# Kernel optimization log

Measured on AMD Instinct MI355X. Metric: run time of the kernel, lower is better.

The kernel has to match this reference:

```python
import jax, jax.numpy as jnp
import numpy as np

UNITS = 400
FEAT = 3
B, T = 128, 1000


def setup_inputs() -> dict:
    key = jax.random.key(0)
    ks = jax.random.split(key, 8)
    s = 0.08  # small init scale
    return {
        "x": jax.random.normal(ks[0], (B, T, FEAT), dtype=jnp.float32),
        "W": jax.random.normal(ks[1], (FEAT, 4 * UNITS), dtype=jnp.float32) * s,
        "U": jax.random.normal(ks[2], (UNITS, 4 * UNITS), dtype=jnp.float32) * s,
        "b": jnp.zeros((4 * UNITS,), dtype=jnp.float32),
        "p_i": jax.random.normal(ks[3], (UNITS,), dtype=jnp.float32) * s,
        "p_f": jax.random.normal(ks[4], (UNITS,), dtype=jnp.float32) * s,
        "p_o": jax.random.normal(ks[5], (UNITS,), dtype=jnp.float32) * s,
        "Wd": jax.random.normal(ks[6], (UNITS, FEAT), dtype=jnp.float32) * s,
        "bd": jnp.zeros((FEAT,), dtype=jnp.float32),
    }


def reference(x, W, U, b, p_i, p_f, p_o, Wd, bd):
    """Peephole LSTM (Graves) scan + dense projection.

    Gate order i, f, g(cell candidate), o. Peepholes: i,f see c_{t-1}; o sees c_t.
    """
    batch = x.shape[0]
    units = U.shape[0]
    # Precompute input contribution for all timesteps: [B, T, 4U]
    xw = jnp.einsum("btf,fg->btg", x, W) + b

    def step(carry, xw_t):
        h, c = carry  # [B, U] each
        z = xw_t + h @ U  # [B, 4U]
        zi, zf, zg, zo = jnp.split(z, 4, axis=-1)
        i = jax.nn.sigmoid(zi + p_i * c)
        f = jax.nn.sigmoid(zf + p_f * c)
        c_new = f * c + i * jnp.tanh(zg)
        o = jax.nn.sigmoid(zo + p_o * c_new)
        h_new = o * jnp.tanh(c_new)
        return (h_new, c_new), h_new

    init = (jnp.zeros((batch, units), x.dtype), jnp.zeros((batch, units), x.dtype))
    _, hs = jax.lax.scan(step, init, jnp.swapaxes(xw, 0, 1))  # hs: [T, B, U]
    hs = jnp.swapaxes(hs, 0, 1)  # [B, T, U]
    return hs @ Wd + bd  # [B, T, FEAT]
```

## Files before the change

kernel.cpp:

```cpp
#include <hip/hip_runtime.h>
#include <hip/hip_bf16.h>

#define UNITS   400
#define BATCH   128
#define TSTEPS  1000
#define NFEAT   3
#define GATES   1600
#define KCAP    448
#define HSTR    456
#define NGROUP  8
#define CWG     20
#define SU      20
#define NCOLS   80
#define ROWS    16
#define NW      5
#define NTHR    320

typedef __bf16 bf16x8 __attribute__((ext_vector_type(8)));
typedef float  v4f    __attribute__((ext_vector_type(4)));

__device__ __forceinline__ float sigm(float v)     { return 1.f / (1.f + __expf(-v)); }
__device__ __forceinline__ float tanhfast(float v) { return 1.f - 2.f / (1.f + __expf(2.f * v)); }

__device__ __forceinline__ unsigned short f2bf(float v) {
    __hip_bfloat16 h = __float2bfloat16(v);
    return *reinterpret_cast<unsigned short*>(&h);
}

__global__ void hw_init_kernel(const float* __restrict__ U, const float* __restrict__ W,
                               const float* __restrict__ b, const float* __restrict__ bd,
                               unsigned short* __restrict__ Urep, float* __restrict__ Wrep,
                               float* __restrict__ brep, unsigned short* __restrict__ Hbuf,
                               int* __restrict__ flags, float* __restrict__ out)
{
    int idx = blockIdx.x * 256 + threadIdx.x;
    if (idx < GATES * KCAP) {
        int col = idx / KCAP, k = idx - col * KCAP;
        int u = col >> 2, G = col & 3;
        float v = (k < UNITS) ? U[k * GATES + G * UNITS + u] : 0.f;
        Urep[idx] = f2bf(v);
        return;
    }
    idx -= GATES * KCAP;
    if (idx < 3 * GATES) {
        int f = idx / GATES, col = idx - f * GATES;
        int u = col >> 2, G = col & 3;
        Wrep[idx] = W[f * GATES + G * UNITS + u];
        return;
    }
    idx -= 3 * GATES;
    if (idx < GATES) {
        int u = idx >> 2, G = idx & 3;
        brep[idx] = b[G * UNITS + u];
        return;
    }
    idx -= GATES;
    if (idx < BATCH * KCAP) { Hbuf[idx] = 0; return; }
    idx -= BATCH * KCAP;
    if (idx < 256) { flags[idx] = 0; return; }
    idx -= 256;
    if (idx < BATCH * TSTEPS * NFEAT) { out[idx] = bd[idx % 3]; return; }
}

__global__ __launch_bounds__(NTHR) void lstm_kernel(
    const float* __restrict__ x,
    const float* __restrict__ p_i, const float* __restrict__ p_f, const float* __restrict__ p_o,
    const float* __restrict__ Wd,
    const unsigned short* __restrict__ Urep,
    const float* __restrict__ Wrep, const float* __restrict__ brep,
    unsigned short* __restrict__ Hbuf,
    int* __restrict__ flags,
    float* __restrict__ out)
{
    __shared__ __align__(16) unsigned short Hl[ROWS * HSTR];
    __shared__ float Wl[3 * NCOLS];
    __shared__ float bl[NCOLS];
    __shared__ float xl[ROWS * 4];
    __shared__ float redw[NW * ROWS * 4];
    float* zb = (float*)Hl;

    const int tid  = threadIdx.x;
    const int lane = tid & 63, wid = tid >> 6;
    const int bid  = blockIdx.x;
    const int grp  = bid & 7;
    const int c    = bid >> 3;
    const int b0   = grp * ROWS;
    const int u0   = c * SU;
    const int col0 = u0 * 4;

    bf16x8 barr[13];
    {
        const int bcol = col0 + wid * 16 + (lane & 15);
        const unsigned short* up = Urep + (size_t)bcol * KCAP + ((lane >> 4) * 8);
        #pragma unroll
        for (int kt = 0; kt < 13; ++kt)
            barr[kt] = *(const bf16x8*)(up + kt * 32);
    }
    for (int i = tid; i < 3 * NCOLS; i += NTHR) {
        int f = i / NCOLS, cl = i - f * NCOLS;
        Wl[i] = Wrep[f * GATES + col0 + cl];
    }
    for (int i = tid; i < NCOLS; i += NTHR) bl[i] = brep[col0 + i];

    const int u   = tid >> 4;
    const int row = tid & 15;
    const int gu  = u0 + u;
    const int gb  = b0 + row;
    const float pi = p_i[gu], pf = p_f[gu], po = p_o[gu];
    const float wd0 = Wd[gu * 3 + 0], wd1 = Wd[gu * 3 + 1], wd2 = Wd[gu * 3 + 2];
    float cst = 0.f;
    int* flagp = flags + grp * 32;

    __syncthreads();

    #pragma unroll 1
    for (int t = 0; t < TSTEPS; ++t) {
        {
            const unsigned long long* src =
                (const unsigned long long*)(Hbuf + (size_t)b0 * KCAP);
            for (int i = tid; i < ROWS * 112; i += NTHR) {
                unsigned long long v = __hip_atomic_load(src + i, __ATOMIC_RELAXED, __HIP_MEMORY_SCOPE_AGENT);
                int r = i / 112, j = i - r * 112;
                *(unsigned long long*)((char*)Hl + r * (HSTR * 2) + j * 8) = v;
            }
            if (tid < 48) {
                int r = tid / 3, f = tid - r * 3;
                xl[r * 4 + f] = x[(size_t)(b0 + r) * (TSTEPS * NFEAT) + t * NFEAT + f];
            }
        }
        __syncthreads();

        v4f acc = {0.f, 0.f, 0.f, 0.f};
        {
            const char* ap = (const char*)Hl + (lane & 15) * (HSTR * 2) + (lane >> 4) * 16;
            #pragma unroll
            for (int kt = 0; kt < 13; ++kt) {
                bf16x8 a = *(const bf16x8*)(ap + kt * 64);
                acc = __builtin_amdgcn_mfma_f32_16x16x32_bf16(a, barr[kt], acc, 0, 0, 0);
            }
        }
        __syncthreads();
        {
            int zc = wid * 16 + (lane & 15);
            int zr = (lane >> 4) * 4;
            #pragma unroll
            for (int j = 0; j < 4; ++j) zb[(zr + j) * NCOLS + zc] = acc[j];
        }
        __syncthreads();

        {
            float x0 = xl[row * 4 + 0], x1 = xl[row * 4 + 1], x2 = xl[row * 4 + 2];
            float z[4];
            #pragma unroll
            for (int G = 0; G < 4; ++G) {
                int cc = u * 4 + G;
                z[G] = zb[row * NCOLS + cc] + bl[cc]
                     + x0 * Wl[0 * NCOLS + cc] + x1 * Wl[1 * NCOLS + cc] + x2 * Wl[2 * NCOLS + cc];
            }
            float iv = sigm(z[0] + pi * cst);
            float fv = sigm(z[1] + pf * cst);
            float cn = fv * cst + iv * tanhfast(z[2]);
            float ov = sigm(z[3] + po * cn);
            float h  = ov * tanhfast(cn);
            cst = cn;

            int hb = (int)f2bf(h);
            int h1 = __shfl_down(hb, 16);
            int h2 = __shfl_down(hb, 32);
            int h3 = __shfl_down(hb, 48);
            if (lane < 16) {
                unsigned int lo = (unsigned int)(hb & 0xffff) | ((unsigned int)(h1 & 0xffff) << 16);
                unsigned int hi = (unsigned int)(h2 & 0xffff) | ((unsigned int)(h3 & 0xffff) << 16);
                unsigned long long pk = (unsigned long long)lo | ((unsigned long long)hi << 32);
                __hip_atomic_store(
                    (unsigned long long*)(Hbuf + (size_t)(b0 + lane) * KCAP + u0 + wid * 4),
                    pk, __ATOMIC_RELAXED, __HIP_MEMORY_SCOPE_AGENT);
            }

            float s0 = h * wd0, s1 = h * wd1, s2 = h * wd2;
            s0 += __shfl_xor(s0, 16); s0 += __shfl_xor(s0, 32);
            s1 += __shfl_xor(s1, 16); s1 += __shfl_xor(s1, 32);
            s2 += __shfl_xor(s2, 16); s2 += __shfl_xor(s2, 32);
            if (lane < 16) {
                redw[(wid * ROWS + lane) * 4 + 0] = s0;
                redw[(wid * ROWS + lane) * 4 + 1] = s1;
                redw[(wid * ROWS + lane) * 4 + 2] = s2;
            }
        }
        __syncthreads();
        if (tid < 48) {
            int f = tid >> 4, r = tid & 15;
            float s = 0.f;
            #pragma unroll
            for (int w2 = 0; w2 < NW; ++w2) s += redw[(w2 * ROWS + r) * 4 + f];
            atomicAdd(&out[(size_t)(b0 + r) * (TSTEPS * NFEAT) + t * NFEAT + f], s);
        }
        __syncthreads();

        if (tid == 0) {
            __hip_atomic_fetch_add(flagp, 1, __ATOMIC_RELAXED, __HIP_MEMORY_SCOPE_AGENT);
            const int target = CWG * (t + 1);
            while (__hip_atomic_load(flagp, __ATOMIC_RELAXED, __HIP_MEMORY_SCOPE_AGENT) < target)
                __builtin_amdgcn_s_sleep(2);
        }
        __syncthreads();
    }
}

extern "C" void kernel_launch(void* const* d_in, const int* in_sizes, int n_in,
                              void* d_out, int out_size, void* d_ws, size_t ws_size,
                              hipStream_t stream)
{
    const float* x   = (const float*)d_in[0];
    const float* W   = (const float*)d_in[1];
    const float* U   = (const float*)d_in[2];
    const float* b   = (const float*)d_in[3];
    const float* p_i = (const float*)d_in[4];
    const float* p_f = (const float*)d_in[5];
    const float* p_o = (const float*)d_in[6];
    const float* Wd  = (const float*)d_in[7];
    const float* bd  = (const float*)d_in[8];
    float* out = (float*)d_out;

    char* p = (char*)d_ws;
    unsigned short* Urep = (unsigned short*)p;  p += (size_t)GATES * KCAP * 2;
    float* Wrep = (float*)p;                    p += (size_t)3 * GATES * 4;
    float* brep = (float*)p;                    p += (size_t)GATES * 4;
    unsigned short* Hbuf = (unsigned short*)p;  p += (size_t)BATCH * KCAP * 2;
    int* flags = (int*)p;                       p += 256 * 4;

    const int total = GATES * KCAP + 3 * GATES + GATES + BATCH * KCAP + 256 + BATCH * TSTEPS * NFEAT;
    const int iblocks = (total + 255) / 256;
    hipLaunchKernelGGL(hw_init_kernel, dim3(iblocks), dim3(256), 0, stream,
                       U, W, b, bd, Urep, Wrep, brep, Hbuf, flags, out);

    hipLaunchKernelGGL(lstm_kernel, dim3(NGROUP * CWG), dim3(NTHR), 0, stream,
                       x, p_i, p_f, p_o, Wd, Urep, Wrep, brep, Hbuf, flags, out);
}
```

Baseline: 3.477 ms.

## Use single-wave blocks with per-wave flags, double-buffered hidden state, and partial output slices

```diff
diff --git a/kernel.cpp b/kernel.cpp
--- a/kernel.cpp
+++ b/kernel.cpp
@@ -4,20 +4,18 @@
 #define UNITS   400
 #define BATCH   128
 #define TSTEPS  1000
-#define NFEAT   3
 #define GATES   1600
 #define KCAP    448
-#define HSTR    456
 #define NGROUP  8
-#define CWG     20
-#define SU      20
-#define NCOLS   80
+#define WPG     100
 #define ROWS    16
-#define NW      5
-#define NTHR    320
+#define OUTSZ   (BATCH*TSTEPS*3)
+#define NSLICE  5
+#define SPIN_GUARD 8192
 
 typedef __bf16 bf16x8 __attribute__((ext_vector_type(8)));
-typedef float  v4f    __attribute__((ext_vector_type(4)));
+typedef float  f32x4  __attribute__((ext_vector_type(4)));
+typedef unsigned long long ull;
 
 __device__ __forceinline__ float sigm(float v)     { return 1.f / (1.f + __expf(-v)); }
 __device__ __forceinline__ float tanhfast(float v) { return 1.f - 2.f / (1.f + __expf(2.f * v)); }
@@ -28,10 +26,10 @@
 }
 
 __global__ void hw_init_kernel(const float* __restrict__ U, const float* __restrict__ W,
-                               const float* __restrict__ b, const float* __restrict__ bd,
+                               const float* __restrict__ b,
                                unsigned short* __restrict__ Urep, float* __restrict__ Wrep,
                                float* __restrict__ brep, unsigned short* __restrict__ Hbuf,
-                               int* __restrict__ flags, float* __restrict__ out)
+                               int* __restrict__ flags, float* __restrict__ outP)
 {
     int idx = blockIdx.x * 256 + threadIdx.x;
     if (idx < GATES * KCAP) {
@@ -55,14 +53,18 @@
         return;
     }
     idx -= GATES;
-    if (idx < BATCH * KCAP) { Hbuf[idx] = 0; return; }
-    idx -= BATCH * KCAP;
-    if (idx < 256) { flags[idx] = 0; return; }
-    idx -= 256;
-    if (idx < BATCH * TSTEPS * NFEAT) { out[idx] = bd[idx % 3]; return; }
-}
-
-__global__ __launch_bounds__(NTHR) void lstm_kernel(
+    if (idx < 2 * BATCH * KCAP) { Hbuf[idx] = 0; return; }
+    idx -= 2 * BATCH * KCAP;
+    if (idx < NGROUP * 128) { flags[idx] = 0; return; }
+    idx -= NGROUP * 128;
+    if (idx < NSLICE * OUTSZ) { outP[idx] = 0.f; return; }
+}
+
+#define LDA(i, offlit) \
+    asm volatile("global_load_dwordx4 %0, %1, off offset:" offlit " sc0 sc1" \
+                 : "=v"(af[i]) : "v"(ab) : "memory");
+
+__global__ __launch_bounds__(64) void lstm_kernel(
     const float* __restrict__ x,
     const float* __restrict__ p_i, const float* __restrict__ p_f, const float* __restrict__ p_o,
     const float* __restrict__ Wd,
@@ -70,141 +72,151 @@
     const float* __restrict__ Wrep, const float* __restrict__ brep,
     unsigned short* __restrict__ Hbuf,
     int* __restrict__ flags,
-    float* __restrict__ out)
-{
-    __shared__ __align__(16) unsigned short Hl[ROWS * HSTR];
-    __shared__ float Wl[3 * NCOLS];
-    __shared__ float bl[NCOLS];
-    __shared__ float xl[ROWS * 4];
-    __shared__ float redw[NW * ROWS * 4];
-    float* zb = (float*)Hl;
-
-    const int tid  = threadIdx.x;
-    const int lane = tid & 63, wid = tid >> 6;
+    float* __restrict__ outP)
+{
+    const int lane = threadIdx.x;
     const int bid  = blockIdx.x;
     const int grp  = bid & 7;
-    const int c    = bid >> 3;
+    const int widx = bid >> 3;
     const int b0   = grp * ROWS;
-    const int u0   = c * SU;
-    const int col0 = u0 * 4;
+    const int ub   = widx * 4;
+    const int col0 = widx * 16;
+    const int row  = lane & 15;
+    const int kg   = lane >> 4;
+    const int gu   = ub + kg;
 
     bf16x8 barr[13];
     {
-        const int bcol = col0 + wid * 16 + (lane & 15);
-        const unsigned short* up = Urep + (size_t)bcol * KCAP + ((lane >> 4) * 8);
+        const unsigned short* up = Urep + (size_t)(col0 + row) * KCAP + kg * 8;
         #pragma unroll
         for (int kt = 0; kt < 13; ++kt)
             barr[kt] = *(const bf16x8*)(up + kt * 32);
     }
-    for (int i = tid; i < 3 * NCOLS; i += NTHR) {
-        int f = i / NCOLS, cl = i - f * NCOLS;
-        Wl[i] = Wrep[f * GATES + col0 + cl];
-    }
-    for (int i = tid; i < NCOLS; i += NTHR) bl[i] = brep[col0 + i];
-
-    const int u   = tid >> 4;
-    const int row = tid & 15;
-    const int gu  = u0 + u;
-    const int gb  = b0 + row;
+
+    float w0[4], w1[4], w2[4], bz[4];
+    #pragma unroll
+    for (int G = 0; G < 4; ++G) {
+        w0[G] = Wrep[0 * GATES + gu * 4 + G];
+        w1[G] = Wrep[1 * GATES + gu * 4 + G];
+        w2[G] = Wrep[2 * GATES + gu * 4 + G];
+        bz[G] = brep[gu * 4 + G];
+    }
     const float pi = p_i[gu], pf = p_f[gu], po = p_o[gu];
     const float wd0 = Wd[gu * 3 + 0], wd1 = Wd[gu * 3 + 1], wd2 = Wd[gu * 3 + 2];
+
+    const size_t bufbytes = (size_t)BATCH * KCAP * 2;
+    const char* arb0 = (const char*)Hbuf + ((size_t)(b0 + row) * KCAP + kg * 8) * 2;
+    const char* arb1 = arb0 + bufbytes;
+    char* awb0 = (char*)Hbuf + ((size_t)(b0 + lane) * KCAP + ub) * 2;
+    char* awb1 = awb0 + bufbytes;
+
+    int* fl    = flags + grp * 128;
+    int* slotp = fl + widx;
+    const float* xp  = x + (size_t)(b0 + row) * (TSTEPS * 3);
+    float* opp = outP + (size_t)(widx % NSLICE) * OUTSZ + (size_t)(b0 + row) * (TSTEPS * 3);
+
+    const int S = ((lane & 12) << 2) + (kg << 2);
+    const int jj = lane & 3;
     float cst = 0.f;
-    int* flagp = flags + grp * 32;
-
-    __syncthreads();
 
     #pragma unroll 1
     for (int t = 0; t < TSTEPS; ++t) {
+        float x0 = xp[t * 3 + 0], x1 = xp[t * 3 + 1], x2 = xp[t * 3 + 2];
+
         {
-            const unsigned long long* src =
-                (const unsigned long long*)(Hbuf + (size_t)b0 * KCAP);
-            for (int i = tid; i < ROWS * 112; i += NTHR) {
-                unsigned long long v = __hip_atomic_load(src + i, __ATOMIC_RELAXED, __HIP_MEMORY_SCOPE_AGENT);
-                int r = i / 112, j = i - r * 112;
-                *(unsigned long long*)((char*)Hl + r * (HSTR * 2) + j * 8) = v;
-            }
-            if (tid < 48) {
-                int r = tid / 3, f = tid - r * 3;
-                xl[r * 4 + f] = x[(size_t)(b0 + r) * (TSTEPS * NFEAT) + t * NFEAT + f];
-            }
-        }
-        __syncthreads();
-
-        v4f acc = {0.f, 0.f, 0.f, 0.f};
+            int f0, f1, guard = 0;
+            bool ok;
+            do {
+                f0 = __hip_atomic_load(fl + lane, __ATOMIC_RELAXED, __HIP_MEMORY_SCOPE_AGENT);
+                f1 = (lane < WPG - 64)
+                     ? __hip_atomic_load(fl + 64 + lane, __ATOMIC_RELAXED, __HIP_MEMORY_SCOPE_AGENT)
+                     : t;
+                ok = __all(f0 >= t && f1 >= t);
+            } while (!ok && ++guard < SPIN_GUARD);
+        }
+
+        f32x4 af[13];
+        const char* ab = (t & 1) ? arb1 : arb0;
+        LDA(0, "0")   LDA(1, "64")  LDA(2, "128") LDA(3, "192")
+        LDA(4, "256") LDA(5, "320") LDA(6, "384") LDA(7, "448")
+        LDA(8, "512") LDA(9, "576") LDA(10, "640") LDA(11, "704") LDA(12, "768")
+        asm volatile("s_waitcnt vmcnt(0)" ::: "memory");
+        __builtin_amdgcn_sched_barrier(0);
+
+        f32x4 a0 = {0.f, 0.f, 0.f, 0.f}, a1 = {0.f, 0.f, 0.f, 0.f};
+        #pragma unroll
+        for (int kt = 0; kt < 13; kt += 2)
+            a0 = __builtin_amdgcn_mfma_f32_16x16x32_bf16(
+                     __builtin_bit_cast(bf16x8, af[kt]), barr[kt], a0, 0, 0, 0);
+        #pragma unroll
+        for (int kt = 1; kt < 13; kt += 2)
+            a1 = __builtin_amdgcn_mfma_f32_16x16x32_bf16(
+                     __builtin_bit_cast(bf16x8, af[kt]), barr[kt], a1, 0, 0, 0);
+        f32x4 acc = a0 + a1;
+
+        float zz[4];
         {
-            const char* ap = (const char*)Hl + (lane & 15) * (HSTR * 2) + (lane >> 4) * 16;
-            #pragma unroll
-            for (int kt = 0; kt < 13; ++kt) {
-                bf16x8 a = *(const bf16x8*)(ap + kt * 64);
-                acc = __builtin_amdgcn_mfma_f32_16x16x32_bf16(a, barr[kt], acc, 0, 0, 0);
-            }
-        }
-        __syncthreads();
-        {
-            int zc = wid * 16 + (lane & 15);
-            int zr = (lane >> 4) * 4;
-            #pragma unroll
-            for (int j = 0; j < 4; ++j) zb[(zr + j) * NCOLS + zc] = acc[j];
-        }
-        __syncthreads();
-
-        {
-            float x0 = xl[row * 4 + 0], x1 = xl[row * 4 + 1], x2 = xl[row * 4 + 2];
-            float z[4];
+            float q0[4], q1[4], q2[4], q3[4];
             #pragma unroll
             for (int G = 0; G < 4; ++G) {
-                int cc = u * 4 + G;
-                z[G] = zb[row * NCOLS + cc] + bl[cc]
-                     + x0 * Wl[0 * NCOLS + cc] + x1 * Wl[1 * NCOLS + cc] + x2 * Wl[2 * NCOLS + cc];
+                q0[G] = __shfl(acc[0], S + G);
+                q1[G] = __shfl(acc[1], S + G);
+                q2[G] = __shfl(acc[2], S + G);
+                q3[G] = __shfl(acc[3], S + G);
             }
-            float iv = sigm(z[0] + pi * cst);
-            float fv = sigm(z[1] + pf * cst);
-            float cn = fv * cst + iv * tanhfast(z[2]);
-            float ov = sigm(z[3] + po * cn);
-            float h  = ov * tanhfast(cn);
-            cst = cn;
-
-            int hb = (int)f2bf(h);
-            int h1 = __shfl_down(hb, 16);
-            int h2 = __shfl_down(hb, 32);
-            int h3 = __shfl_down(hb, 48);
-            if (lane < 16) {
-                unsigned int lo = (unsigned int)(hb & 0xffff) | ((unsigned int)(h1 & 0xffff) << 16);
-                unsigned int hi = (unsigned int)(h2 & 0xffff) | ((unsigned int)(h3 & 0xffff) << 16);
-                unsigned long long pk = (unsigned long long)lo | ((unsigned long long)hi << 32);
-                __hip_atomic_store(
-                    (unsigned long long*)(Hbuf + (size_t)(b0 + lane) * KCAP + u0 + wid * 4),
-                    pk, __ATOMIC_RELAXED, __HIP_MEMORY_SCOPE_AGENT);
+            #pragma unroll
+            for (int G = 0; G < 4; ++G) {
+                float r = q0[G];
+                r = (jj == 1) ? q1[G] : r;
+                r = (jj == 2) ? q2[G] : r;
+                r = (jj == 3) ? q3[G] : r;
+                zz[G] = r + bz[G] + x0 * w0[G] + x1 * w1[G] + x2 * w2[G];
             }
-
-            float s0 = h * wd0, s1 = h * wd1, s2 = h * wd2;
-            s0 += __shfl_xor(s0, 16); s0 += __shfl_xor(s0, 32);
-            s1 += __shfl_xor(s1, 16); s1 += __shfl_xor(s1, 32);
-            s2 += __shfl_xor(s2, 16); s2 += __shfl_xor(s2, 32);
-            if (lane < 16) {
-                redw[(wid * ROWS + lane) * 4 + 0] = s0;
-                redw[(wid * ROWS + lane) * 4 + 1] = s1;
-                redw[(wid * ROWS + lane) * 4 + 2] = s2;
-            }
-        }
-        __syncthreads();
-        if (tid < 48) {
-            int f = tid >> 4, r = tid & 15;
-            float s = 0.f;
-            #pragma unroll
-            for (int w2 = 0; w2 < NW; ++w2) s += redw[(w2 * ROWS + r) * 4 + f];
-            atomicAdd(&out[(size_t)(b0 + r) * (TSTEPS * NFEAT) + t * NFEAT + f], s);
-        }
-        __syncthreads();
-
-        if (tid == 0) {
-            __hip_atomic_fetch_add(flagp, 1, __ATOMIC_RELAXED, __HIP_MEMORY_SCOPE_AGENT);
-            const int target = CWG * (t + 1);
-            while (__hip_atomic_load(flagp, __ATOMIC_RELAXED, __HIP_MEMORY_SCOPE_AGENT) < target)
-                __builtin_amdgcn_s_sleep(2);
-        }
-        __syncthreads();
-    }
+        }
+
+        float iv = sigm(zz[0] + pi * cst);
+        float fv = sigm(zz[1] + pf * cst);
+        float cn = fv * cst + iv * tanhfast(zz[2]);
+        float ov = sigm(zz[3] + po * cn);
+        float h  = ov * tanhfast(cn);
+        cst = cn;
+
+        int hb = (int)f2bf(h);
+        int h1 = __shfl_down(hb, 16);
+        int h2 = __shfl_down(hb, 32);
+        int h3 = __shfl_down(hb, 48);
+        if (lane < 16) {
+            unsigned int lo = (unsigned int)(hb & 0xffff) | ((unsigned int)(h1 & 0xffff) << 16);
+            unsigned int hi = (unsigned int)(h2 & 0xffff) | ((unsigned int)(h3 & 0xffff) << 16);
+            ull pk = (ull)lo | ((ull)hi << 32);
+            ull* dst = (ull*)((t & 1) ? awb0 : awb1);
+            __hip_atomic_store(dst, pk, __ATOMIC_RELAXED, __HIP_MEMORY_SCOPE_AGENT);
+        }
+        asm volatile("s_waitcnt vmcnt(0)" ::: "memory");
+        if (lane == 0)
+            __hip_atomic_store(slotp, t + 1, __ATOMIC_RELAXED, __HIP_MEMORY_SCOPE_AGENT);
+
+        float s0 = h * wd0, s1 = h * wd1, s2 = h * wd2;
+        s0 += __shfl_xor(s0, 16); s0 += __shfl_xor(s0, 32);
+        s1 += __shfl_xor(s1, 16); s1 += __shfl_xor(s1, 32);
+        s2 += __shfl_xor(s2, 16); s2 += __shfl_xor(s2, 32);
+        if (lane < 16) {
+            atomicAdd(opp + t * 3 + 0, s0);
+            atomicAdd(opp + t * 3 + 1, s1);
+            atomicAdd(opp + t * 3 + 2, s2);
+        }
+    }
+}
+
+__global__ void merge_kernel(const float* __restrict__ outP, const float* __restrict__ bd,
+                             float* __restrict__ out)
+{
+    int i = blockIdx.x * 256 + threadIdx.x;
+    if (i >= OUTSZ) return;
+    float s = bd[i % 3];
+    #pragma unroll
+    for (int k = 0; k < NSLICE; ++k) s += outP[(size_t)k * OUTSZ + i];
+    out[i] = s;
 }
 
 extern "C" void kernel_launch(void* const* d_in, const int* in_sizes, int n_in,
@@ -226,14 +238,19 @@
     unsigned short* Urep = (unsigned short*)p;  p += (size_t)GATES * KCAP * 2;
     float* Wrep = (float*)p;                    p += (size_t)3 * GATES * 4;
     float* brep = (float*)p;                    p += (size_t)GATES * 4;
-    unsigned short* Hbuf = (unsigned short*)p;  p += (size_t)BATCH * KCAP * 2;
-    int* flags = (int*)p;                       p += 256 * 4;
-
-    const int total = GATES * KCAP + 3 * GATES + GATES + BATCH * KCAP + 256 + BATCH * TSTEPS * NFEAT;
+    unsigned short* Hbuf = (unsigned short*)p;  p += (size_t)2 * BATCH * KCAP * 2;
+    int* flags = (int*)p;                       p += (size_t)NGROUP * 128 * 4;
+    float* outP = (float*)p;                    p += (size_t)NSLICE * OUTSZ * 4;
+
+    const int total = GATES * KCAP + 3 * GATES + GATES + 2 * BATCH * KCAP
+                    + NGROUP * 128 + NSLICE * OUTSZ;
     const int iblocks = (total + 255) / 256;
     hipLaunchKernelGGL(hw_init_kernel, dim3(iblocks), dim3(256), 0, stream,
-                       U, W, b, bd, Urep, Wrep, brep, Hbuf, flags, out);
-
-    hipLaunchKernelGGL(lstm_kernel, dim3(NGROUP * CWG), dim3(NTHR), 0, stream,
-                       x, p_i, p_f, p_o, Wd, Urep, Wrep, brep, Hbuf, flags, out);
-}
+                       U, W, b, Urep, Wrep, brep, Hbuf, flags, outP);
+
+    hipLaunchKernelGGL(lstm_kernel, dim3(NGROUP * WPG), dim3(64), 0, stream,
+                       x, p_i, p_f, p_o, Wd, Urep, Wrep, brep, Hbuf, flags, outP);
+
+    hipLaunchKernelGGL(merge_kernel, dim3((OUTSZ + 255) / 256), dim3(256), 0, stream,
+                       outP, bd, out);
+}
```

Measured after the change: 9.555 ms. +174.8%, slower.
